# Kernel tuning notes

Measured on AMD Instinct MI355X. Metric: run time of the kernel, lower is better.

The kernel has to match this reference:

```python
import jax, jax.numpy as jnp
import numpy as np

C_PAIR = 128
N_TOK = 512
EPS = 1e-5


def _layernorm(x, w, b):
    mu = jnp.mean(x, axis=-1, keepdims=True)
    var = jnp.mean(jnp.square(x - mu), axis=-1, keepdims=True)
    return (x - mu) * jax.lax.rsqrt(var + EPS) * w + b


def setup_inputs() -> dict:
    key = jax.random.key(0)
    ks = jax.random.split(key, 8)
    c = C_PAIR
    pair = jax.random.normal(ks[0], (N_TOK, N_TOK, c), dtype=jnp.float32)
    mask = jax.random.uniform(ks[1], (N_TOK, N_TOK), dtype=jnp.float32)
    s_in = 1.0 / np.sqrt(c)
    W_proj = jax.random.normal(ks[2], (2 * c, c), dtype=jnp.float32) * s_in  # nn.Linear(c, 2c)
    W_gate = jax.random.normal(ks[3], (2 * c, c), dtype=jnp.float32) * s_in
    W_out = jax.random.normal(ks[4], (c, c), dtype=jnp.float32) * s_in
    W_glin = jax.random.normal(ks[5], (c, c), dtype=jnp.float32) * s_in
    ln1_w = jnp.ones((c,), jnp.float32)
    ln1_b = jnp.zeros((c,), jnp.float32)
    ln2_w = jnp.ones((c,), jnp.float32)
    ln2_b = jnp.zeros((c,), jnp.float32)
    return {"pair": pair, "mask": mask, "ln1_w": ln1_w, "ln1_b": ln1_b,
            "ln2_w": ln2_w, "ln2_b": ln2_b, "W_proj": W_proj, "W_gate": W_gate,
            "W_out": W_out, "W_glin": W_glin}


def reference(pair, mask, ln1_w, ln1_b, ln2_w, ln2_b, W_proj, W_gate, W_out, W_glin):
    # pair: [N, N, c], mask: [N, N]
    x = _layernorm(pair, ln1_w, ln1_b)
    input_pair = x
    proj = x @ W_proj.T                      # [N, N, 2c]
    proj = proj * mask[..., None]
    gate = x @ W_gate.T                      # [N, N, 2c]
    proj = proj * jax.nn.sigmoid(gate)
    # torch reshape(2c,...)->(c,2,...) then chunk: a = channels 0::2, b = channels 1::2
    a = proj[..., 0::2]                      # [N, N, c]
    b = proj[..., 1::2]                      # [N, N, c]
    # equation 'ckj,cki->cij' in channel-first == out[i,j,c] = sum_k a[k,j,c] * b[k,i,c]
    out = jnp.einsum('kjc,kic->ijc', a, b)   # [N, N, c]
    out = _layernorm(out, ln2_w, ln2_b)
    out = out @ W_out.T
    gate_out = input_pair @ W_glin.T
    return out * jax.nn.sigmoid(gate_out)
```

## Files before the change

kernel.cpp:

```cpp
#include <hip/hip_runtime.h>
#include <hip/hip_bf16.h>

using u16 = unsigned short;
typedef __attribute__((ext_vector_type(4))) float f32x4;
typedef __attribute__((ext_vector_type(8))) _Float16 f16x8;
typedef __attribute__((ext_vector_type(4))) unsigned short u16x4;
typedef __attribute__((ext_vector_type(8))) unsigned short u16x8;

#define MFMA(a,b,c) __builtin_amdgcn_mfma_f32_16x16x32_f16((a),(b),(c),0,0,0)

__device__ __forceinline__ u16 f2h(float f){
  _Float16 h = (_Float16)f;
  return __builtin_bit_cast(u16, h);
}
__device__ __forceinline__ float sigm(float x){
  return 1.f / (1.f + __expf(-x));
}
__device__ __forceinline__ f16x8 ldw8(const float* __restrict__ W, int row, int koff){
  const float4* p = (const float4*)(W + row * 128 + koff);
  float4 f0 = p[0], f1 = p[1];
  f16x8 h;
  h[0] = (_Float16)f0.x; h[1] = (_Float16)f0.y; h[2] = (_Float16)f0.z; h[3] = (_Float16)f0.w;
  h[4] = (_Float16)f1.x; h[5] = (_Float16)f1.y; h[6] = (_Float16)f1.z; h[7] = (_Float16)f1.w;
  return h;
}

__launch_bounds__(256, 3)
__global__ void k1_ln_proj(const float* __restrict__ pair, const float* __restrict__ mask,
                           const float* __restrict__ ln1w, const float* __restrict__ ln1b,
                           const float* __restrict__ Wp, const float* __restrict__ Wg,
                           u16* __restrict__ a_r, u16* __restrict__ b_r){
  __shared__ float red_s[128], red_q[128], msk[128];
  __shared__ u16 xs[128 * 136];
  __shared__ u16 sbuf[4][16 * 132];
  int tid = threadIdx.x;
  int bid = blockIdx.x;
  int j   = bid >> 2;
  int k0  = (bid & 3) << 7;

  int cpos = tid & 31;
  int rsub = tid >> 5;
  float4 v[16];
  #pragma unroll
  for (int it = 0; it < 16; ++it){
    int kk = it * 8 + rsub;
    const float4* p = (const float4*)(pair + (((size_t)(k0 + kk) * 512 + j) << 7));
    v[it] = p[cpos];
    float s = v[it].x + v[it].y + v[it].z + v[it].w;
    float q = v[it].x*v[it].x + v[it].y*v[it].y + v[it].z*v[it].z + v[it].w*v[it].w;
    #pragma unroll
    for (int m = 16; m >= 1; m >>= 1){
      s += __shfl_xor(s, m);
      q += __shfl_xor(q, m);
    }
    if (cpos == 0){ red_s[kk] = s; red_q[kk] = q; }
  }
  if (tid < 128) msk[tid] = mask[(size_t)(k0 + tid) * 512 + j];
  __syncthreads();

  float4 w4 = ((const float4*)ln1w)[cpos];
  float4 b4 = ((const float4*)ln1b)[cpos];
  #pragma unroll
  for (int it = 0; it < 16; ++it){
    int kk = it * 8 + rsub;
    float mu = red_s[kk] * (1.f / 128.f);
    float var = red_q[kk] * (1.f / 128.f) - mu * mu;
    float rs = rsqrtf(var + 1e-5f);
    u16x4 o;
    o[0] = f2h((v[it].x - mu) * rs * w4.x + b4.x);
    o[1] = f2h((v[it].y - mu) * rs * w4.y + b4.y);
    o[2] = f2h((v[it].z - mu) * rs * w4.z + b4.z);
    o[3] = f2h((v[it].w - mu) * rs * w4.w + b4.w);
    *(u16x4*)&xs[kk * 136 + cpos * 4] = o;
  }
  __syncthreads();

  int lane = tid & 63;
  int wv   = tid >> 6;
  int l15  = lane & 15;
  int l4   = lane >> 4;
  u16* sb  = sbuf[wv];

  #pragma unroll
  for (int pi = 0; pi < 4; ++pi){
    int tp = pi * 4 + wv;
    int nP = tp * 16 + l15;
    f32x4 accP[8] = {}; f32x4 accG[8] = {};
    #pragma unroll
    for (int ks = 0; ks < 4; ++ks){
      f16x8 bP = ldw8(Wp, nP, ks * 32 + l4 * 8);
      f16x8 bG = ldw8(Wg, nP, ks * 32 + l4 * 8);
      #pragma unroll
      for (int mi = 0; mi < 8; ++mi){
        f16x8 af = *(const f16x8*)&xs[(mi * 16 + l15) * 136 + ks * 32 + l4 * 8];
        accP[mi] = MFMA(af, bP, accP[mi]);
        accG[mi] = MFMA(af, bG, accG[mi]);
      }
    }
    #pragma unroll
    for (int mi = 0; mi < 8; ++mi){
      int m0 = mi * 16 + l4 * 4;
      u16x4 o;
      #pragma unroll
      for (int r = 0; r < 4; ++r){
        float p = accP[mi][r] * msk[m0 + r] * sigm(accG[mi][r]);
        o[r] = f2h(p);
      }
      *(u16x4*)&sb[l15 * 132 + m0] = o;
    }
    #pragma unroll
    for (int r2 = 0; r2 < 8; ++r2){
      int row = r2 * 2 + (lane >> 5);
      int col = (lane & 31) * 4;
      u16x4 vv = *(const u16x4*)&sb[row * 132 + col];
      int nP2 = tp * 16 + row;
      int c = nP2 >> 1;
      u16* dst = (nP2 & 1) ? b_r : a_r;
      *(u16x4*)&dst[((size_t)c * 512 + j) * 512 + k0 + col] = vv;
    }
  }
}

__launch_bounds__(256, 2)
__global__ void k2_tri(const u16* __restrict__ a_r, const u16* __restrict__ b_r,
                       float* __restrict__ o_f){
  int tid = threadIdx.x;
  int p = blockIdx.x;
  int lb = (p & 7) * 256 + (p >> 3);
  int c  = lb >> 4;
  int t  = lb & 15;
  int lane = tid & 63, wv = tid >> 6;
  int i0 = (t >> 2) * 128 + (wv >> 1) * 64;
  int j0 = (t & 3) * 128 + (wv & 1) * 64;
  int l15 = lane & 15, l4 = lane >> 4;
  const u16* pa = a_r + (size_t)c * 262144;
  const u16* pb = b_r + (size_t)c * 262144;

  f32x4 acc[4][4] = {};
  for (int ks = 0; ks < 16; ++ks){
    f16x8 A[4], B[4];
    #pragma unroll
    for (int ai = 0; ai < 4; ++ai)
      A[ai] = *(const f16x8*)&pb[(i0 + ai * 16 + l15) * 512 + ks * 32 + l4 * 8];
    #pragma unroll
    for (int bj = 0; bj < 4; ++bj)
      B[bj] = *(const f16x8*)&pa[(j0 + bj * 16 + l15) * 512 + ks * 32 + l4 * 8];
    #pragma unroll
    for (int ai = 0; ai < 4; ++ai)
      #pragma unroll
      for (int bj = 0; bj < 4; ++bj)
        acc[ai][bj] = MFMA(A[ai], B[bj], acc[ai][bj]);
  }
  float* po = o_f + (size_t)c * 262144;
  #pragma unroll
  for (int ai = 0; ai < 4; ++ai){
    #pragma unroll
    for (int r = 0; r < 4; ++r){
      int i = i0 + ai * 16 + l4 * 4 + r;
      #pragma unroll
      for (int bj = 0; bj < 4; ++bj)
        po[i * 512 + j0 + bj * 16 + l15] = acc[ai][bj][r];
    }
  }
}

__launch_bounds__(256, 4)
__global__ void k2b_lnt(const float* __restrict__ o_f,
                        const float* __restrict__ ln2w, const float* __restrict__ ln2b,
                        u16* __restrict__ x2g){
  __shared__ float sred[2][4][16][4];
  __shared__ float mu_s[64], rs_s[64];
  __shared__ u16 tr2[64 * 132];
  int tid = threadIdx.x;
  size_t t0 = (size_t)blockIdx.x * 64;
  int part = tid & 15;
  int grp  = tid >> 4;
  int wv = tid >> 6, lane = tid & 63;

  f32x4 vals[8];
  float s4[4] = {0,0,0,0}, q4[4] = {0,0,0,0};
  #pragma unroll
  for (int it = 0; it < 8; ++it){
    int ci = it * 16 + grp;
    vals[it] = *(const f32x4*)&o_f[(size_t)ci * 262144 + t0 + part * 4];
    #pragma unroll
    for (int r = 0; r < 4; ++r){ s4[r] += vals[it][r]; q4[r] += vals[it][r]*vals[it][r]; }
  }
  #pragma unroll
  for (int r = 0; r < 4; ++r){
    s4[r] += __shfl_xor(s4[r], 16); q4[r] += __shfl_xor(q4[r], 16);
    s4[r] += __shfl_xor(s4[r], 32); q4[r] += __shfl_xor(q4[r], 32);
  }
  if (lane < 16){
    #pragma unroll
    for (int r = 0; r < 4; ++r){ sred[0][wv][lane][r] = s4[r]; sred[1][wv][lane][r] = q4[r]; }
  }
  __syncthreads();
  if (tid < 64){
    float s = 0.f, q = 0.f;
    #pragma unroll
    for (int w = 0; w < 4; ++w){ s += sred[0][w][tid >> 2][tid & 3]; q += sred[1][w][tid >> 2][tid & 3]; }
    float mu = s * (1.f / 128.f);
    float var = q * (1.f / 128.f) - mu * mu;
    mu_s[tid] = mu;
    rs_s[tid] = rsqrtf(var + 1e-5f);
  }
  __syncthreads();
  #pragma unroll
  for (int it = 0; it < 8; ++it){
    int ci = it * 16 + grp;
    float w2 = ln2w[ci], b2 = ln2b[ci];
    #pragma unroll
    for (int r = 0; r < 4; ++r){
      int tl = part * 4 + r;
      tr2[tl * 132 + ci] = f2h((vals[it][r] - mu_s[tl]) * rs_s[tl] * w2 + b2);
    }
  }
  __syncthreads();
  #pragma unroll
  for (int it = 0; it < 4; ++it){
    int flat = it * 256 + tid;
    int t = flat >> 4, ch = flat & 15;
    u16x4 lo = *(const u16x4*)&tr2[t * 132 + ch * 8];
    u16x4 hi = *(const u16x4*)&tr2[t * 132 + ch * 8 + 4];
    u16x8 o;
    o[0]=lo[0]; o[1]=lo[1]; o[2]=lo[2]; o[3]=lo[3];
    o[4]=hi[0]; o[5]=hi[1]; o[6]=hi[2]; o[7]=hi[3];
    *(u16x8*)&x2g[(t0 + t) * 128 + ch * 8] = o;
  }
}

__launch_bounds__(256, 4)
__global__ void k3_out(const u16* __restrict__ x2g, const float* __restrict__ pair,
                       const float* __restrict__ ln1w, const float* __restrict__ ln1b,
                       const float* __restrict__ Wgl, const float* __restrict__ Wo,
                       float* __restrict__ out){
  __shared__ u16 x1[64 * 136];
  __shared__ float r1s[64], r1q[64];
  int tid = threadIdx.x, bid = blockIdx.x;
  int i  = bid >> 3;
  int j0 = (bid & 7) << 6;

  int cq = tid & 31, jsub = tid >> 5;
  float4 pv[8];
  #pragma unroll
  for (int it = 0; it < 8; ++it){
    int jj = it * 8 + jsub;
    const float4* p = (const float4*)(pair + (((size_t)i * 512 + j0 + jj) << 7));
    pv[it] = p[cq];
    float s = pv[it].x + pv[it].y + pv[it].z + pv[it].w;
    float q = pv[it].x*pv[it].x + pv[it].y*pv[it].y + pv[it].z*pv[it].z + pv[it].w*pv[it].w;
    #pragma unroll
    for (int m = 16; m >= 1; m >>= 1){
      s += __shfl_xor(s, m);
      q += __shfl_xor(q, m);
    }
    if (cq == 0){ r1s[jj] = s; r1q[jj] = q; }
  }
  __syncthreads();
  {
    float4 w1 = ((const float4*)ln1w)[cq];
    float4 b1 = ((const float4*)ln1b)[cq];
    #pragma unroll
    for (int it = 0; it < 8; ++it){
      int jj = it * 8 + jsub;
      float mu = r1s[jj] * (1.f / 128.f);
      float var = r1q[jj] * (1.f / 128.f) - mu * mu;
      float rs = rsqrtf(var + 1e-5f);
      u16x4 o;
      o[0] = f2h((pv[it].x - mu) * rs * w1.x + b1.x);
      o[1] = f2h((pv[it].y - mu) * rs * w1.y + b1.y);
      o[2] = f2h((pv[it].z - mu) * rs * w1.z + b1.z);
      o[3] = f2h((pv[it].w - mu) * rs * w1.w + b1.w);
      *(u16x4*)&x1[jj * 136 + cq * 4] = o;
    }
  }
  __syncthreads();

  int lane = tid & 63, wv = tid >> 6;
  int l15 = lane & 15, l4 = lane >> 4;
  int n0 = wv * 32;
  f32x4 accO[4][2] = {};
  f32x4 accG[4][2] = {};
  #pragma unroll
  for (int ks = 0; ks < 4; ++ks){
    int koff = ks * 32 + l4 * 8;
    f16x8 B0 = ldw8(Wo, n0 + l15, koff);
    f16x8 B1 = ldw8(Wo, n0 + 16 + l15, koff);
    f16x8 G0 = ldw8(Wgl, n0 + l15, koff);
    f16x8 G1 = ldw8(Wgl, n0 + 16 + l15, koff);
    #pragma unroll
    for (int mi = 0; mi < 4; ++mi){
      f16x8 A2 = *(const f16x8*)&x2g[((size_t)i * 512 + j0 + mi * 16 + l15) * 128 + koff];
      f16x8 A1 = *(const f16x8*)&x1[(mi * 16 + l15) * 136 + koff];
      accO[mi][0] = MFMA(A2, B0, accO[mi][0]);
      accO[mi][1] = MFMA(A2, B1, accO[mi][1]);
      accG[mi][0] = MFMA(A1, G0, accG[mi][0]);
      accG[mi][1] = MFMA(A1, G1, accG[mi][1]);
    }
  }
  #pragma unroll
  for (int mi = 0; mi < 4; ++mi){
    #pragma unroll
    for (int r = 0; r < 4; ++r){
      int m = mi * 16 + l4 * 4 + r;
      size_t tok = (size_t)i * 512 + j0 + m;
      #pragma unroll
      for (int nj = 0; nj < 2; ++nj){
        int cout = n0 + nj * 16 + l15;
        out[tok * 128 + cout] = accO[mi][nj][r] * sigm(accG[mi][nj][r]);
      }
    }
  }
}

extern "C" void kernel_launch(void* const* d_in, const int* in_sizes, int n_in,
                              void* d_out, int out_size, void* d_ws, size_t ws_size,
                              hipStream_t stream){
  (void)in_sizes; (void)n_in; (void)out_size; (void)ws_size;
  const float* pair = (const float*)d_in[0];
  const float* mask = (const float*)d_in[1];
  const float* ln1w = (const float*)d_in[2];
  const float* ln1b = (const float*)d_in[3];
  const float* ln2w = (const float*)d_in[4];
  const float* ln2b = (const float*)d_in[5];
  const float* Wp   = (const float*)d_in[6];
  const float* Wg   = (const float*)d_in[7];
  const float* Wo   = (const float*)d_in[8];
  const float* Wgl  = (const float*)d_in[9];
  float* out = (float*)d_out;

  char* ws = (char*)d_ws;
  u16*   a_r = (u16*)(ws);
  u16*   b_r = (u16*)(ws + 67108864);
  float* o_f = (float*)(ws + 134217728);
  u16*   x2g = (u16*)(ws);

  hipLaunchKernelGGL(k1_ln_proj, dim3(2048), dim3(256), 0, stream, pair, mask, ln1w, ln1b, Wp, Wg, a_r, b_r);
  hipLaunchKernelGGL(k2_tri,     dim3(2048), dim3(256), 0, stream, a_r, b_r, o_f);
  hipLaunchKernelGGL(k2b_lnt,    dim3(4096), dim3(256), 0, stream, o_f, ln2w, ln2b, x2g);
  hipLaunchKernelGGL(k3_out,     dim3(4096), dim3(256), 0, stream, x2g, pair, ln1w, ln1b, Wgl, Wo, out);
}
```

Measured before the change: 451.6 us.

## Fold LN1 into gate weights in output kernel and drop LDS staging passes

The output kernel no longer normalizes pair tokens through shared memory. It feeds raw fp16 pair values into the gate MFMA with ln1 weights folded into W_glin, then applies the row mean/rstd correction algebraically after accumulation using per-row sums gathered during the K loop. The projection kernel drops its LDS transpose buffer and writes the output directly with narrower scattered stores. The LN2 kernel is reorganized for contiguous channel groups with vector LDS writes and reads, and launch bounds are retuned. Raw fp16 pair inputs without centering risk some precision loss, and the direct stores in k1 are less coalesced.

```diff
diff --git a/kernel.cpp b/kernel.cpp
--- a/kernel.cpp
+++ b/kernel.cpp
@@ -25,14 +25,13 @@
   return h;
 }
 
-__launch_bounds__(256, 3)
+__launch_bounds__(256, 4)
 __global__ void k1_ln_proj(const float* __restrict__ pair, const float* __restrict__ mask,
                            const float* __restrict__ ln1w, const float* __restrict__ ln1b,
                            const float* __restrict__ Wp, const float* __restrict__ Wg,
                            u16* __restrict__ a_r, u16* __restrict__ b_r){
   __shared__ float red_s[128], red_q[128], msk[128];
   __shared__ u16 xs[128 * 136];
-  __shared__ u16 sbuf[4][16 * 132];
   int tid = threadIdx.x;
   int bid = blockIdx.x;
   int j   = bid >> 2;
@@ -79,7 +78,6 @@
   int wv   = tid >> 6;
   int l15  = lane & 15;
   int l4   = lane >> 4;
-  u16* sb  = sbuf[wv];
 
   #pragma unroll
   for (int pi = 0; pi < 4; ++pi){
@@ -97,6 +95,9 @@
         accG[mi] = MFMA(af, bG, accG[mi]);
       }
     }
+    int c = nP >> 1;
+    u16* dst = (nP & 1) ? b_r : a_r;
+    size_t base = ((size_t)c * 512 + j) * 512 + k0;
     #pragma unroll
     for (int mi = 0; mi < 8; ++mi){
       int m0 = mi * 16 + l4 * 4;
@@ -106,17 +107,7 @@
         float p = accP[mi][r] * msk[m0 + r] * sigm(accG[mi][r]);
         o[r] = f2h(p);
       }
-      *(u16x4*)&sb[l15 * 132 + m0] = o;
-    }
-    #pragma unroll
-    for (int r2 = 0; r2 < 8; ++r2){
-      int row = r2 * 2 + (lane >> 5);
-      int col = (lane & 31) * 4;
-      u16x4 vv = *(const u16x4*)&sb[row * 132 + col];
-      int nP2 = tp * 16 + row;
-      int c = nP2 >> 1;
-      u16* dst = (nP2 & 1) ? b_r : a_r;
-      *(u16x4*)&dst[((size_t)c * 512 + j) * 512 + k0 + col] = vv;
+      *(u16x4*)&dst[base + m0] = o;
     }
   }
 }
@@ -164,25 +155,25 @@
   }
 }
 
-__launch_bounds__(256, 4)
+__launch_bounds__(256, 6)
 __global__ void k2b_lnt(const float* __restrict__ o_f,
                         const float* __restrict__ ln2w, const float* __restrict__ ln2b,
                         u16* __restrict__ x2g){
   __shared__ float sred[2][4][16][4];
   __shared__ float mu_s[64], rs_s[64];
-  __shared__ u16 tr2[64 * 132];
+  __shared__ u16 tr2[64 * 136];
   int tid = threadIdx.x;
   size_t t0 = (size_t)blockIdx.x * 64;
   int part = tid & 15;
   int grp  = tid >> 4;
+  int ci0  = grp * 8;
   int wv = tid >> 6, lane = tid & 63;
 
   f32x4 vals[8];
   float s4[4] = {0,0,0,0}, q4[4] = {0,0,0,0};
   #pragma unroll
   for (int it = 0; it < 8; ++it){
-    int ci = it * 16 + grp;
-    vals[it] = *(const f32x4*)&o_f[(size_t)ci * 262144 + t0 + part * 4];
+    vals[it] = *(const f32x4*)&o_f[(size_t)(ci0 + it) * 262144 + t0 + part * 4];
     #pragma unroll
     for (int r = 0; r < 4; ++r){ s4[r] += vals[it][r]; q4[r] += vals[it][r]*vals[it][r]; }
   }
@@ -206,14 +197,22 @@
     rs_s[tid] = rsqrtf(var + 1e-5f);
   }
   __syncthreads();
-  #pragma unroll
-  for (int it = 0; it < 8; ++it){
-    int ci = it * 16 + grp;
-    float w2 = ln2w[ci], b2 = ln2b[ci];
+  {
+    float4 w2a = *(const float4*)(ln2w + ci0);
+    float4 w2b = *(const float4*)(ln2w + ci0 + 4);
+    float4 b2a = *(const float4*)(ln2b + ci0);
+    float4 b2b = *(const float4*)(ln2b + ci0 + 4);
+    float w2[8] = {w2a.x,w2a.y,w2a.z,w2a.w,w2b.x,w2b.y,w2b.z,w2b.w};
+    float b2[8] = {b2a.x,b2a.y,b2a.z,b2a.w,b2b.x,b2b.y,b2b.z,b2b.w};
     #pragma unroll
     for (int r = 0; r < 4; ++r){
       int tl = part * 4 + r;
-      tr2[tl * 132 + ci] = f2h((vals[it][r] - mu_s[tl]) * rs_s[tl] * w2 + b2);
+      float mu = mu_s[tl], rs = rs_s[tl];
+      u16x8 o;
+      #pragma unroll
+      for (int it = 0; it < 8; ++it)
+        o[it] = f2h((vals[it][r] - mu) * rs * w2[it] + b2[it]);
+      *(u16x8*)&tr2[tl * 136 + ci0] = o;
     }
   }
   __syncthreads();
@@ -221,95 +220,106 @@
   for (int it = 0; it < 4; ++it){
     int flat = it * 256 + tid;
     int t = flat >> 4, ch = flat & 15;
-    u16x4 lo = *(const u16x4*)&tr2[t * 132 + ch * 8];
-    u16x4 hi = *(const u16x4*)&tr2[t * 132 + ch * 8 + 4];
-    u16x8 o;
-    o[0]=lo[0]; o[1]=lo[1]; o[2]=lo[2]; o[3]=lo[3];
-    o[4]=hi[0]; o[5]=hi[1]; o[6]=hi[2]; o[7]=hi[3];
+    u16x8 o = *(const u16x8*)&tr2[t * 136 + ch * 8];
     *(u16x8*)&x2g[(t0 + t) * 128 + ch * 8] = o;
   }
 }
 
-__launch_bounds__(256, 4)
+__launch_bounds__(256, 3)
 __global__ void k3_out(const u16* __restrict__ x2g, const float* __restrict__ pair,
                        const float* __restrict__ ln1w, const float* __restrict__ ln1b,
                        const float* __restrict__ Wgl, const float* __restrict__ Wo,
                        float* __restrict__ out){
-  __shared__ u16 x1[64 * 136];
-  __shared__ float r1s[64], r1q[64];
   int tid = threadIdx.x, bid = blockIdx.x;
   int i  = bid >> 3;
   int j0 = (bid & 7) << 6;
-
-  int cq = tid & 31, jsub = tid >> 5;
-  float4 pv[8];
-  #pragma unroll
-  for (int it = 0; it < 8; ++it){
-    int jj = it * 8 + jsub;
-    const float4* p = (const float4*)(pair + (((size_t)i * 512 + j0 + jj) << 7));
-    pv[it] = p[cq];
-    float s = pv[it].x + pv[it].y + pv[it].z + pv[it].w;
-    float q = pv[it].x*pv[it].x + pv[it].y*pv[it].y + pv[it].z*pv[it].z + pv[it].w*pv[it].w;
-    #pragma unroll
-    for (int m = 16; m >= 1; m >>= 1){
-      s += __shfl_xor(s, m);
-      q += __shfl_xor(q, m);
-    }
-    if (cq == 0){ r1s[jj] = s; r1q[jj] = q; }
-  }
-  __syncthreads();
-  {
-    float4 w1 = ((const float4*)ln1w)[cq];
-    float4 b1 = ((const float4*)ln1b)[cq];
-    #pragma unroll
-    for (int it = 0; it < 8; ++it){
-      int jj = it * 8 + jsub;
-      float mu = r1s[jj] * (1.f / 128.f);
-      float var = r1q[jj] * (1.f / 128.f) - mu * mu;
-      float rs = rsqrtf(var + 1e-5f);
-      u16x4 o;
-      o[0] = f2h((pv[it].x - mu) * rs * w1.x + b1.x);
-      o[1] = f2h((pv[it].y - mu) * rs * w1.y + b1.y);
-      o[2] = f2h((pv[it].z - mu) * rs * w1.z + b1.z);
-      o[3] = f2h((pv[it].w - mu) * rs * w1.w + b1.w);
-      *(u16x4*)&x1[jj * 136 + cq * 4] = o;
-    }
-  }
-  __syncthreads();
-
   int lane = tid & 63, wv = tid >> 6;
   int l15 = lane & 15, l4 = lane >> 4;
   int n0 = wv * 32;
+
   f32x4 accO[4][2] = {};
   f32x4 accG[4][2] = {};
+  float sA[4] = {0,0,0,0}, qA[4] = {0,0,0,0};
+  float sS0 = 0.f, sS1 = 0.f, sB0 = 0.f, sB1 = 0.f;
+
   #pragma unroll
   for (int ks = 0; ks < 4; ++ks){
     int koff = ks * 32 + l4 * 8;
+    float4 w1a = *(const float4*)(ln1w + koff);
+    float4 w1b = *(const float4*)(ln1w + koff + 4);
+    float4 b1a = *(const float4*)(ln1b + koff);
+    float4 b1b = *(const float4*)(ln1b + koff + 4);
+
+    f16x8 G0, G1;
+    {
+      const float4* p = (const float4*)(Wgl + (n0 + l15) * 128 + koff);
+      float4 f0 = p[0], f1 = p[1];
+      float e0=f0.x*w1a.x, e1=f0.y*w1a.y, e2=f0.z*w1a.z, e3=f0.w*w1a.w;
+      float e4=f1.x*w1b.x, e5=f1.y*w1b.y, e6=f1.z*w1b.z, e7=f1.w*w1b.w;
+      G0[0]=(_Float16)e0; G0[1]=(_Float16)e1; G0[2]=(_Float16)e2; G0[3]=(_Float16)e3;
+      G0[4]=(_Float16)e4; G0[5]=(_Float16)e5; G0[6]=(_Float16)e6; G0[7]=(_Float16)e7;
+      sS0 += (e0+e1+e2+e3)+(e4+e5+e6+e7);
+      sB0 += f0.x*b1a.x + f0.y*b1a.y + f0.z*b1a.z + f0.w*b1a.w
+           + f1.x*b1b.x + f1.y*b1b.y + f1.z*b1b.z + f1.w*b1b.w;
+    }
+    {
+      const float4* p = (const float4*)(Wgl + (n0 + 16 + l15) * 128 + koff);
+      float4 f0 = p[0], f1 = p[1];
+      float e0=f0.x*w1a.x, e1=f0.y*w1a.y, e2=f0.z*w1a.z, e3=f0.w*w1a.w;
+      float e4=f1.x*w1b.x, e5=f1.y*w1b.y, e6=f1.z*w1b.z, e7=f1.w*w1b.w;
+      G1[0]=(_Float16)e0; G1[1]=(_Float16)e1; G1[2]=(_Float16)e2; G1[3]=(_Float16)e3;
+      G1[4]=(_Float16)e4; G1[5]=(_Float16)e5; G1[6]=(_Float16)e6; G1[7]=(_Float16)e7;
+      sS1 += (e0+e1+e2+e3)+(e4+e5+e6+e7);
+      sB1 += f0.x*b1a.x + f0.y*b1a.y + f0.z*b1a.z + f0.w*b1a.w
+           + f1.x*b1b.x + f1.y*b1b.y + f1.z*b1b.z + f1.w*b1b.w;
+    }
     f16x8 B0 = ldw8(Wo, n0 + l15, koff);
     f16x8 B1 = ldw8(Wo, n0 + 16 + l15, koff);
-    f16x8 G0 = ldw8(Wgl, n0 + l15, koff);
-    f16x8 G1 = ldw8(Wgl, n0 + 16 + l15, koff);
+
     #pragma unroll
     for (int mi = 0; mi < 4; ++mi){
-      f16x8 A2 = *(const f16x8*)&x2g[((size_t)i * 512 + j0 + mi * 16 + l15) * 128 + koff];
-      f16x8 A1 = *(const f16x8*)&x1[(mi * 16 + l15) * 136 + koff];
+      size_t row = (size_t)i * 512 + j0 + mi * 16 + l15;
+      f16x8 A2 = *(const f16x8*)&x2g[row * 128 + koff];
+      const float4* pp = (const float4*)(pair + row * 128 + koff);
+      float4 x0 = pp[0], x1 = pp[1];
+      f16x8 A1;
+      A1[0]=(_Float16)x0.x; A1[1]=(_Float16)x0.y; A1[2]=(_Float16)x0.z; A1[3]=(_Float16)x0.w;
+      A1[4]=(_Float16)x1.x; A1[5]=(_Float16)x1.y; A1[6]=(_Float16)x1.z; A1[7]=(_Float16)x1.w;
+      sA[mi] += (x0.x+x0.y+x0.z+x0.w) + (x1.x+x1.y+x1.z+x1.w);
+      qA[mi] += x0.x*x0.x + x0.y*x0.y + x0.z*x0.z + x0.w*x0.w
+              + x1.x*x1.x + x1.y*x1.y + x1.z*x1.z + x1.w*x1.w;
       accO[mi][0] = MFMA(A2, B0, accO[mi][0]);
       accO[mi][1] = MFMA(A2, B1, accO[mi][1]);
       accG[mi][0] = MFMA(A1, G0, accG[mi][0]);
       accG[mi][1] = MFMA(A1, G1, accG[mi][1]);
     }
   }
+
   #pragma unroll
   for (int mi = 0; mi < 4; ++mi){
+    sA[mi] += __shfl_xor(sA[mi], 16); sA[mi] += __shfl_xor(sA[mi], 32);
+    qA[mi] += __shfl_xor(qA[mi], 16); qA[mi] += __shfl_xor(qA[mi], 32);
+  }
+  sS0 += __shfl_xor(sS0, 16); sS0 += __shfl_xor(sS0, 32);
+  sS1 += __shfl_xor(sS1, 16); sS1 += __shfl_xor(sS1, 32);
+  sB0 += __shfl_xor(sB0, 16); sB0 += __shfl_xor(sB0, 32);
+  sB1 += __shfl_xor(sB1, 16); sB1 += __shfl_xor(sB1, 32);
+
+  #pragma unroll
+  for (int mi = 0; mi < 4; ++mi){
+    float mu_r = sA[mi] * (1.f / 128.f);
+    float rs_r = rsqrtf(qA[mi] * (1.f / 128.f) - mu_r * mu_r + 1e-5f);
     #pragma unroll
     for (int r = 0; r < 4; ++r){
+      int srcl = (lane & 48) | (l4 * 4 + r);
+      float mu = __shfl(mu_r, srcl);
+      float rs = __shfl(rs_r, srcl);
       int m = mi * 16 + l4 * 4 + r;
       size_t tok = (size_t)i * 512 + j0 + m;
-      #pragma unroll
-      for (int nj = 0; nj < 2; ++nj){
-        int cout = n0 + nj * 16 + l15;
-        out[tok * 128 + cout] = accO[mi][nj][r] * sigm(accG[mi][nj][r]);
-      }
+      float g0 = rs * (accG[mi][0][r] - mu * sS0) + sB0;
+      float g1 = rs * (accG[mi][1][r] - mu * sS1) + sB1;
+      out[tok * 128 + n0 + l15]      = accO[mi][0][r] * sigm(g0);
+      out[tok * 128 + n0 + 16 + l15] = accO[mi][1][r] * sigm(g1);
     }
   }
 }
```

Measured after the change: 698.9 us. +54.8%, slower.
